# Optimization experiments

Hardware: AMD Instinct MI355X
Metric: run time of the kernel (lower is better)

Reference implementation:

```python
import jax, jax.numpy as jnp
import numpy as np

B, OBS, A, T, E, H = 2048, 1024, 512, 64, 16, 64


def setup_inputs() -> dict:
    key = jax.random.key(0)
    ks = jax.random.split(key, 20)
    w = lambda k, shp, s=0.05: (jax.random.normal(k, shp, dtype=jnp.float32) * s)
    x = jax.random.normal(ks[0], (B, OBS), dtype=jnp.float32)
    action_types = jax.random.randint(ks[1], (B, A), 0, T, dtype=jnp.int32)
    # valid action counts in [1, A] so no env has an empty (all -inf) logit row
    action_counts = jax.random.randint(ks[2], (B,), 1, A + 1, dtype=jnp.int32)
    # sampled action must index a valid (unmasked) logit
    action = jnp.mod(jax.random.randint(ks[3], (B,), 0, A, dtype=jnp.int32), action_counts)
    return {
        "x": x, "action_types": action_types, "action_counts": action_counts, "action": action,
        "emb": w(ks[4], (T, E)),
        # actor_base: obs->64->64, tanh
        "W1": w(ks[5], (OBS, H)), "b1": jnp.zeros((H,), jnp.float32),
        "W2": w(ks[6], (H, H)), "b2": jnp.zeros((H,), jnp.float32),
        # action_head first linear split: [feat(64) | embed(16)] -> 64
        "Wf": w(ks[7], (H, H)), "We": w(ks[8], (E, H)), "ba": jnp.zeros((H,), jnp.float32),
        "Wo": w(ks[9], (H, 1), 0.01), "bo": jnp.zeros((1,), jnp.float32),
        # critic: obs->64->64->1, tanh
        "Wc1": w(ks[10], (OBS, H)), "bc1": jnp.zeros((H,), jnp.float32),
        "Wc2": w(ks[11], (H, H)), "bc2": jnp.zeros((H,), jnp.float32),
        "Wc3": w(ks[12], (H, 1), 1.0), "bc3": jnp.zeros((1,), jnp.float32),
    }


def reference(x, action_types, action_counts, action, emb, W1, b1, W2, b2,
              Wf, We, ba, Wo, bo, Wc1, bc1, Wc2, bc2, Wc3, bc3):
    # actor_base features [B,H]
    feats = jnp.tanh(jnp.tanh(x @ W1 + b1) @ W2 + b2)
    # ragged action scoring, padded to [B,A]:
    # combined = cat(feats_broadcast, embed(action_types)); first linear split as Wf/We
    ae = emb[action_types]                                   # [B,A,E]
    h = jnp.tanh((feats @ Wf)[:, None, :] + jnp.einsum('bae,eh->bah', ae, We) + ba)  # [B,A,H]
    scores = jnp.einsum('bah,h->ba', h, Wo[:, 0]) + bo[0]    # [B,A]
    mask = jnp.arange(A, dtype=jnp.int32)[None, :] < action_counts[:, None]
    logits = jnp.where(mask, scores, -jnp.inf)
    logp = jax.nn.log_softmax(logits, axis=-1)               # [B,A]
    log_prob = jnp.take_along_axis(logp, action[:, None].astype(jnp.int32), axis=1)[:, 0]
    p = jnp.exp(logp)
    entropy = -jnp.sum(jnp.where(mask, p * logp, 0.0), axis=-1)
    # critic value [B,1]
    value = jnp.tanh(jnp.tanh(x @ Wc1 + bc1) @ Wc2 + bc2) @ Wc3 + bc3
    return jnp.stack([log_prob, entropy, value[:, 0]], axis=-1)  # [B,3]
```

## Files before the change

### kernel.cpp

```cpp
#include <hip/hip_runtime.h>
#include <hip/hip_bf16.h>

#define B_    2048
#define OBS_  1024
#define A_    512
#define NC    128
#define NSLICE 8
#define PADK  136

typedef __attribute__((ext_vector_type(8))) short bf16x8;
typedef __attribute__((ext_vector_type(4))) float f32x4;

__device__ __forceinline__ float fast_tanh(float x) {
    return 1.0f - 2.0f / (__expf(2.0f * x) + 1.0f);
}

__device__ __forceinline__ unsigned short rne_bf16(float f) {
    union { float f; unsigned u; } v; v.f = f;
    unsigned u = v.u;
    return (unsigned short)((u + 0x7FFFu + ((u >> 16) & 1u)) >> 16);
}

__device__ __forceinline__ unsigned pack_bf16(float lo, float hi) {
    return (unsigned)rne_bf16(lo) | ((unsigned)rne_bf16(hi) << 16);
}

__device__ __forceinline__ short to_bf16(float f) {
    __hip_bfloat16 h = __float2bfloat16(f);
    return *reinterpret_cast<short*>(&h);
}

#define RL(x, k) __int_as_float(__builtin_amdgcn_readlane(__float_as_int(x), (k)))

#define WS_VTP   0
#define WS_W2P   8192
#define WS_WFP   16384
#define WS_WC2P  24576
#define WS_PART  32768

__global__ __launch_bounds__(256) void k1_mfma(
        const float* __restrict__ x, const float* __restrict__ W1,
        const float* __restrict__ Wc1, const float* __restrict__ emb,
        const float* __restrict__ We, const float* __restrict__ W2,
        const float* __restrict__ Wf, const float* __restrict__ Wc2,
        unsigned char* __restrict__ ws) {
    __shared__ unsigned short wT[128 * PADK];
    const int tid    = threadIdx.x;
    const int bid    = blockIdx.x;
    const int mb     = bid >> 3;
    const int kslice = bid & 7;
    const int k0     = kslice * 128;

    {
        const int n  = tid & 127;
        const int th = tid >> 7;
        const float* src = (n < 64) ? (W1 + n) : (Wc1 + (n - 64));
        #pragma unroll
        for (int gg = 0; gg < 16; ++gg) {
            int kq = gg * 2 + th;
            int k  = k0 + kq * 4;
            float w0 = src[(size_t)(k + 0) * 64];
            float w1 = src[(size_t)(k + 1) * 64];
            float w2 = src[(size_t)(k + 2) * 64];
            float w3 = src[(size_t)(k + 3) * 64];
            unsigned long long v = (unsigned long long)pack_bf16(w0, w1)
                                 | ((unsigned long long)pack_bf16(w2, w3) << 32);
            *reinterpret_cast<unsigned long long*>(&wT[n * PADK + kq * 4]) = v;
        }
    }
    __syncthreads();

    const int w = tid >> 6;
    const int l = tid & 63;
    const int c = l & 15;
    const int g = l >> 4;

    const float* xrow0 = x + (size_t)(mb * 32 + c) * OBS_ + k0 + g * 8;
    const float* xrow1 = xrow0 + (size_t)16 * OBS_;
    const int nt0 = 2 * w, nt1 = 2 * w + 1;
    const unsigned short* bp0 = &wT[(nt0 * 16 + c) * PADK + g * 8];
    const unsigned short* bp1 = &wT[(nt1 * 16 + c) * PADK + g * 8];

    f32x4 acc00 = {0.f, 0.f, 0.f, 0.f};
    f32x4 acc01 = {0.f, 0.f, 0.f, 0.f};
    f32x4 acc10 = {0.f, 0.f, 0.f, 0.f};
    f32x4 acc11 = {0.f, 0.f, 0.f, 0.f};
    #pragma unroll
    for (int ks = 0; ks < 4; ++ks) {
        const float4* xp0 = (const float4*)(xrow0 + ks * 32);
        const float4* xp1 = (const float4*)(xrow1 + ks * 32);
        float4 a0 = xp0[0], a1 = xp0[1];
        float4 b0 = xp1[0], b1 = xp1[1];
        bf16x8 av0, av1;
        av0[0] = to_bf16(a0.x); av0[1] = to_bf16(a0.y);
        av0[2] = to_bf16(a0.z); av0[3] = to_bf16(a0.w);
        av0[4] = to_bf16(a1.x); av0[5] = to_bf16(a1.y);
        av0[6] = to_bf16(a1.z); av0[7] = to_bf16(a1.w);
        av1[0] = to_bf16(b0.x); av1[1] = to_bf16(b0.y);
        av1[2] = to_bf16(b0.z); av1[3] = to_bf16(b0.w);
        av1[4] = to_bf16(b1.x); av1[5] = to_bf16(b1.y);
        av1[6] = to_bf16(b1.z); av1[7] = to_bf16(b1.w);
        bf16x8 bv0 = *(const bf16x8*)(bp0 + ks * 32);
        bf16x8 bv1 = *(const bf16x8*)(bp1 + ks * 32);
        acc00 = __builtin_amdgcn_mfma_f32_16x16x32_bf16(av0, bv0, acc00, 0, 0, 0);
        acc01 = __builtin_amdgcn_mfma_f32_16x16x32_bf16(av0, bv1, acc01, 0, 0, 0);
        acc10 = __builtin_amdgcn_mfma_f32_16x16x32_bf16(av1, bv0, acc10, 0, 0, 0);
        acc11 = __builtin_amdgcn_mfma_f32_16x16x32_bf16(av1, bv1, acc11, 0, 0, 0);
    }

    float* pbase = (float*)(ws + WS_PART) + (size_t)kslice * B_ * NC;
    const int col0 = nt0 * 16 + c;
    const int col1 = nt1 * 16 + c;
    const int r0   = mb * 32 + g * 4;
    const int r1   = r0 + 16;
    #pragma unroll
    for (int r = 0; r < 4; ++r) {
        pbase[(size_t)(r0 + r) * NC + col0] = acc00[r];
        pbase[(size_t)(r0 + r) * NC + col1] = acc01[r];
        pbase[(size_t)(r1 + r) * NC + col0] = acc10[r];
        pbase[(size_t)(r1 + r) * NC + col1] = acc11[r];
    }

    if (bid < 32) {
        const int job = bid >> 3;
        const int idx = (bid & 7) * 256 + tid;
        if (job == 0) {
            int hp = idx >> 6, t = idx & 63;
            float s0 = 0.f, s1 = 0.f;
            #pragma unroll
            for (int e = 0; e < 16; ++e) {
                float ev = emb[t * 16 + e];
                s0 += ev * We[e * 64 + 2 * hp];
                s1 += ev * We[e * 64 + 2 * hp + 1];
            }
            ((unsigned*)(ws + WS_VTP))[idx] = pack_bf16(s0, s1);
        } else {
            const float* src = (job == 1) ? W2 : (job == 2) ? Wf : Wc2;
            unsigned* dst = (unsigned*)(ws + ((job == 1) ? WS_W2P : (job == 2) ? WS_WFP : WS_WC2P));
            int rp = idx >> 6, hh = idx & 63;
            dst[idx] = pack_bf16(src[(2 * rp) * 64 + hh], src[(2 * rp + 1) * 64 + hh]);
        }
    }
}

__global__ __launch_bounds__(256) void k2_score(
        const unsigned char* __restrict__ ws,
        const int* __restrict__ action_types, const int* __restrict__ action_counts,
        const int* __restrict__ action,
        const float* __restrict__ b1, const float* __restrict__ bc1,
        const float* __restrict__ b2, const float* __restrict__ ba,
        const float* __restrict__ Wo, const float* __restrict__ bo,
        const float* __restrict__ bc2, const float* __restrict__ Wc3,
        const float* __restrict__ bc3, float* __restrict__ out) {
    __shared__ unsigned sW2p[32][64];
    __shared__ unsigned sWfp[32][64];
    __shared__ unsigned sWc2p[32][64];
    __shared__ unsigned sVTp[32][64];
    __shared__ int scnt[4][64];

    const int tid = threadIdx.x;
    {
        const unsigned* gV = (const unsigned*)(ws + WS_VTP);
        const unsigned* g2 = (const unsigned*)(ws + WS_W2P);
        const unsigned* gF = (const unsigned*)(ws + WS_WFP);
        const unsigned* gC = (const unsigned*)(ws + WS_WC2P);
        #pragma unroll
        for (int i = 0; i < 8; ++i) {
            int idx = tid + i * 256;
            ((unsigned*)sVTp)[idx]  = gV[idx];
            ((unsigned*)sW2p)[idx]  = g2[idx];
            ((unsigned*)sWfp)[idx]  = gF[idx];
            ((unsigned*)sWc2p)[idx] = gC[idx];
        }
    }
    scnt[tid >> 6][tid & 63] = 0;
    __syncthreads();

    const int lane = tid & 63;
    const int wid  = tid >> 6;
    const int b    = blockIdx.x * 4 + wid;

    const float* pa = (const float*)(ws + WS_PART) + (size_t)b * NC + lane;
    float h1v = 0.f, c1v = 0.f;
    #pragma unroll
    for (int s8 = 0; s8 < NSLICE; ++s8) {
        h1v += pa[(size_t)s8 * B_ * NC];
        c1v += pa[(size_t)s8 * B_ * NC + 64];
    }
    h1v = fast_tanh(h1v + b1[lane]);
    c1v = fast_tanh(c1v + bc1[lane]);
    const int* at_row = action_types + (size_t)b * A_;
    const int count = action_counts[b];
    const int base = lane * 8;
    int4 p0 = *reinterpret_cast<const int4*>(at_row + base);
    int4 p1 = *reinterpret_cast<const int4*>(at_row + base + 4);
    const int a_star = action[b];
    const int t_star = at_row[a_star] & 63;

    float f = b2[lane];
    #pragma unroll
    for (int kp = 0; kp < 32; ++kp) {
        unsigned pw = sW2p[kp][lane];
        f += RL(h1v, 2 * kp)     * __uint_as_float(pw << 16);
        f += RL(h1v, 2 * kp + 1) * __uint_as_float(pw & 0xffff0000u);
    }
    f = fast_tanh(f);

    float u = ba[lane];
    #pragma unroll
    for (int kp = 0; kp < 32; ++kp) {
        unsigned pw = sWfp[kp][lane];
        u += RL(f, 2 * kp)     * __uint_as_float(pw << 16);
        u += RL(f, 2 * kp + 1) * __uint_as_float(pw & 0xffff0000u);
    }

    float cc = bc2[lane];
    #pragma unroll
    for (int kp = 0; kp < 32; ++kp) {
        unsigned pw = sWc2p[kp][lane];
        cc += RL(c1v, 2 * kp)     * __uint_as_float(pw << 16);
        cc += RL(c1v, 2 * kp + 1) * __uint_as_float(pw & 0xffff0000u);
    }
    cc = fast_tanh(cc);
    float pv = cc * Wc3[lane];
    #pragma unroll
    for (int off = 32; off > 0; off >>= 1) pv += __shfl_xor(pv, off);
    const float value = pv + bc3[0];

    float s = bo[0];
    #pragma unroll
    for (int hp = 0; hp < 32; ++hp) {
        unsigned pvv = sVTp[hp][lane];
        s += fast_tanh(RL(u, 2 * hp)     + __uint_as_float(pvv << 16))         * Wo[2 * hp];
        s += fast_tanh(RL(u, 2 * hp + 1) + __uint_as_float(pvv & 0xffff0000u)) * Wo[2 * hp + 1];
    }

    int* cptr = scnt[wid];
    if (base + 0 < count) atomicAdd(&cptr[p0.x & 63], 1);
    if (base + 1 < count) atomicAdd(&cptr[p0.y & 63], 1);
    if (base + 2 < count) atomicAdd(&cptr[p0.z & 63], 1);
    if (base + 3 < count) atomicAdd(&cptr[p0.w & 63], 1);
    if (base + 4 < count) atomicAdd(&cptr[p1.x & 63], 1);
    if (base + 5 < count) atomicAdd(&cptr[p1.y & 63], 1);
    if (base + 6 < count) atomicAdd(&cptr[p1.z & 63], 1);
    if (base + 7 < count) atomicAdd(&cptr[p1.w & 63], 1);

    const int cv = cptr[lane];
    float mval = (cv > 0) ? s : -3.0e38f;
    #pragma unroll
    for (int off = 32; off > 0; off >>= 1) mval = fmaxf(mval, __shfl_xor(mval, off));
    const float e  = (float)cv * __expf(s - mval);
    float se = e, sd = e * s;
    #pragma unroll
    for (int off = 32; off > 0; off >>= 1) {
        se += __shfl_xor(se, off);
        sd += __shfl_xor(sd, off);
    }
    const float logZ    = mval + __logf(se);
    const float entropy = logZ - sd / se;
    const float logp    = __shfl(s, t_star) - logZ;

    if (lane == 0) {
        out[b * 3 + 0] = logp;
        out[b * 3 + 1] = entropy;
        out[b * 3 + 2] = value;
    }
}

extern "C" void kernel_launch(void* const* d_in, const int* in_sizes, int n_in,
                              void* d_out, int out_size, void* d_ws, size_t ws_size,
                              hipStream_t stream) {
    const float* x             = (const float*)d_in[0];
    const int*   action_types  = (const int*)  d_in[1];
    const int*   action_counts = (const int*)  d_in[2];
    const int*   action        = (const int*)  d_in[3];
    const float* emb           = (const float*)d_in[4];
    const float* W1            = (const float*)d_in[5];
    const float* b1            = (const float*)d_in[6];
    const float* W2            = (const float*)d_in[7];
    const float* b2            = (const float*)d_in[8];
    const float* Wf            = (const float*)d_in[9];
    const float* We            = (const float*)d_in[10];
    const float* ba            = (const float*)d_in[11];
    const float* Wo            = (const float*)d_in[12];
    const float* bo            = (const float*)d_in[13];
    const float* Wc1           = (const float*)d_in[14];
    const float* bc1           = (const float*)d_in[15];
    const float* Wc2           = (const float*)d_in[16];
    const float* bc2           = (const float*)d_in[17];
    const float* Wc3           = (const float*)d_in[18];
    const float* bc3           = (const float*)d_in[19];
    float* out = (float*)d_out;
    unsigned char* ws = (unsigned char*)d_ws;

    k1_mfma<<<512, 256, 0, stream>>>(x, W1, Wc1, emb, We, W2, Wf, Wc2, ws);
    k2_score<<<512, 256, 0, stream>>>(ws, action_types, action_counts, action,
                                      b1, bc1, b2, ba, Wo, bo, bc2, Wc3, bc3, out);
}
```

Before: 26.71 us.

## Store split-K partials as bf16 in row-major slice layout; split accumulator chains

The first kernel now writes its split-K partial sums as bf16 instead of fp32, and places all slices of a row next to each other. This halves workspace traffic and keeps the second kernel's per-batch reads local. The small matvec and scoring loops in the second kernel now use four independent accumulators instead of one, shortening dependent FMA chains. Rounding the partials to bf16 adds precision loss before the tanh.

```diff
diff --git a/kernel.cpp b/kernel.cpp
--- a/kernel.cpp
+++ b/kernel.cpp
@@ -29,6 +29,10 @@
     __hip_bfloat16 h = __float2bfloat16(f);
     return *reinterpret_cast<short*>(&h);
 }
+
+__device__ __forceinline__ float bf16_lo(unsigned p) { return __uint_as_float(p << 16); }
+__device__ __forceinline__ float bf16_hi(unsigned p) { return __uint_as_float(p & 0xffff0000u); }
+__device__ __forceinline__ float bf16_f(unsigned short v) { return __uint_as_float(((unsigned)v) << 16); }
 
 #define RL(x, k) __int_as_float(__builtin_amdgcn_readlane(__float_as_int(x), (k)))
 
@@ -108,17 +112,17 @@
         acc11 = __builtin_amdgcn_mfma_f32_16x16x32_bf16(av1, bv1, acc11, 0, 0, 0);
     }
 
-    float* pbase = (float*)(ws + WS_PART) + (size_t)kslice * B_ * NC;
+    unsigned short* pbase = (unsigned short*)(ws + WS_PART);
     const int col0 = nt0 * 16 + c;
     const int col1 = nt1 * 16 + c;
     const int r0   = mb * 32 + g * 4;
     const int r1   = r0 + 16;
     #pragma unroll
     for (int r = 0; r < 4; ++r) {
-        pbase[(size_t)(r0 + r) * NC + col0] = acc00[r];
-        pbase[(size_t)(r0 + r) * NC + col1] = acc01[r];
-        pbase[(size_t)(r1 + r) * NC + col0] = acc10[r];
-        pbase[(size_t)(r1 + r) * NC + col1] = acc11[r];
+        pbase[((size_t)(r0 + r) * NSLICE + kslice) * NC + col0] = (unsigned short)to_bf16(acc00[r]);
+        pbase[((size_t)(r0 + r) * NSLICE + kslice) * NC + col1] = (unsigned short)to_bf16(acc01[r]);
+        pbase[((size_t)(r1 + r) * NSLICE + kslice) * NC + col0] = (unsigned short)to_bf16(acc10[r]);
+        pbase[((size_t)(r1 + r) * NSLICE + kslice) * NC + col1] = (unsigned short)to_bf16(acc11[r]);
     }
 
     if (bid < 32) {
@@ -180,15 +184,19 @@
     const int wid  = tid >> 6;
     const int b    = blockIdx.x * 4 + wid;
 
-    const float* pa = (const float*)(ws + WS_PART) + (size_t)b * NC + lane;
-    float h1v = 0.f, c1v = 0.f;
-    #pragma unroll
-    for (int s8 = 0; s8 < NSLICE; ++s8) {
-        h1v += pa[(size_t)s8 * B_ * NC];
-        c1v += pa[(size_t)s8 * B_ * NC + 64];
-    }
-    h1v = fast_tanh(h1v + b1[lane]);
-    c1v = fast_tanh(c1v + bc1[lane]);
+    const unsigned short* pa = (const unsigned short*)(ws + WS_PART)
+                             + (size_t)b * NSLICE * NC + lane;
+    float h1a = 0.f, h1b = 0.f, c1a = 0.f, c1b = 0.f;
+    #pragma unroll
+    for (int s8 = 0; s8 < NSLICE; s8 += 2) {
+        h1a += bf16_f(pa[s8 * NC]);
+        h1b += bf16_f(pa[(s8 + 1) * NC]);
+        c1a += bf16_f(pa[s8 * NC + 64]);
+        c1b += bf16_f(pa[(s8 + 1) * NC + 64]);
+    }
+    float h1v = fast_tanh(h1a + h1b + b1[lane]);
+    float c1v = fast_tanh(c1a + c1b + bc1[lane]);
+
     const int* at_row = action_types + (size_t)b * A_;
     const int count = action_counts[b];
     const int base = lane * 8;
@@ -197,43 +205,57 @@
     const int a_star = action[b];
     const int t_star = at_row[a_star] & 63;
 
-    float f = b2[lane];
-    #pragma unroll
-    for (int kp = 0; kp < 32; ++kp) {
-        unsigned pw = sW2p[kp][lane];
-        f += RL(h1v, 2 * kp)     * __uint_as_float(pw << 16);
-        f += RL(h1v, 2 * kp + 1) * __uint_as_float(pw & 0xffff0000u);
-    }
-    f = fast_tanh(f);
-
-    float u = ba[lane];
-    #pragma unroll
-    for (int kp = 0; kp < 32; ++kp) {
-        unsigned pw = sWfp[kp][lane];
-        u += RL(f, 2 * kp)     * __uint_as_float(pw << 16);
-        u += RL(f, 2 * kp + 1) * __uint_as_float(pw & 0xffff0000u);
-    }
-
-    float cc = bc2[lane];
-    #pragma unroll
-    for (int kp = 0; kp < 32; ++kp) {
-        unsigned pw = sWc2p[kp][lane];
-        cc += RL(c1v, 2 * kp)     * __uint_as_float(pw << 16);
-        cc += RL(c1v, 2 * kp + 1) * __uint_as_float(pw & 0xffff0000u);
-    }
-    cc = fast_tanh(cc);
+    float f0 = b2[lane], f1 = 0.f, f2 = 0.f, f3 = 0.f;
+    #pragma unroll
+    for (int kp = 0; kp < 32; kp += 2) {
+        unsigned pwA = sW2p[kp][lane];
+        unsigned pwB = sW2p[kp + 1][lane];
+        f0 += RL(h1v, 2 * kp)     * bf16_lo(pwA);
+        f1 += RL(h1v, 2 * kp + 1) * bf16_hi(pwA);
+        f2 += RL(h1v, 2 * kp + 2) * bf16_lo(pwB);
+        f3 += RL(h1v, 2 * kp + 3) * bf16_hi(pwB);
+    }
+    const float f = fast_tanh((f0 + f1) + (f2 + f3));
+
+    float u0 = ba[lane], u1 = 0.f, u2 = 0.f, u3 = 0.f;
+    #pragma unroll
+    for (int kp = 0; kp < 32; kp += 2) {
+        unsigned pwA = sWfp[kp][lane];
+        unsigned pwB = sWfp[kp + 1][lane];
+        u0 += RL(f, 2 * kp)     * bf16_lo(pwA);
+        u1 += RL(f, 2 * kp + 1) * bf16_hi(pwA);
+        u2 += RL(f, 2 * kp + 2) * bf16_lo(pwB);
+        u3 += RL(f, 2 * kp + 3) * bf16_hi(pwB);
+    }
+    const float u = (u0 + u1) + (u2 + u3);
+
+    float g0 = bc2[lane], g1 = 0.f, g2 = 0.f, g3 = 0.f;
+    #pragma unroll
+    for (int kp = 0; kp < 32; kp += 2) {
+        unsigned pwA = sWc2p[kp][lane];
+        unsigned pwB = sWc2p[kp + 1][lane];
+        g0 += RL(c1v, 2 * kp)     * bf16_lo(pwA);
+        g1 += RL(c1v, 2 * kp + 1) * bf16_hi(pwA);
+        g2 += RL(c1v, 2 * kp + 2) * bf16_lo(pwB);
+        g3 += RL(c1v, 2 * kp + 3) * bf16_hi(pwB);
+    }
+    float cc = fast_tanh((g0 + g1) + (g2 + g3));
     float pv = cc * Wc3[lane];
     #pragma unroll
     for (int off = 32; off > 0; off >>= 1) pv += __shfl_xor(pv, off);
     const float value = pv + bc3[0];
 
-    float s = bo[0];
-    #pragma unroll
-    for (int hp = 0; hp < 32; ++hp) {
-        unsigned pvv = sVTp[hp][lane];
-        s += fast_tanh(RL(u, 2 * hp)     + __uint_as_float(pvv << 16))         * Wo[2 * hp];
-        s += fast_tanh(RL(u, 2 * hp + 1) + __uint_as_float(pvv & 0xffff0000u)) * Wo[2 * hp + 1];
-    }
+    float s0 = bo[0], s1 = 0.f, s2 = 0.f, s3 = 0.f;
+    #pragma unroll
+    for (int hp = 0; hp < 32; hp += 2) {
+        unsigned pvA = sVTp[hp][lane];
+        unsigned pvB = sVTp[hp + 1][lane];
+        s0 += fast_tanh(RL(u, 2 * hp)     + bf16_lo(pvA)) * Wo[2 * hp];
+        s1 += fast_tanh(RL(u, 2 * hp + 1) + bf16_hi(pvA)) * Wo[2 * hp + 1];
+        s2 += fast_tanh(RL(u, 2 * hp + 2) + bf16_lo(pvB)) * Wo[2 * hp + 2];
+        s3 += fast_tanh(RL(u, 2 * hp + 3) + bf16_hi(pvB)) * Wo[2 * hp + 3];
+    }
+    const float s = (s0 + s1) + (s2 + s3);
 
     int* cptr = scnt[wid];
     if (base + 0 < count) atomicAdd(&cptr[p0.x & 63], 1);
```

Result: faster. 24.68 us (-7.6%).
